# Kernel optimization log

Hardware: AMD Instinct MI355X
Metric: run time of the kernel (lower is better)

Reference implementation:

```python
import jax, jax.numpy as jnp
import numpy as np

SHAPE_MIN = -1.0
SHAPE_LENGTH = 2.0
RESOLUTION = 128
EPS = 1e-05

# plane -> coordinate dims picked by normalize_coordinate
PLANE_DIMS = {"xy": (0, 1), "yz": (1, 2), "xz": (0, 2)}


def setup_inputs() -> dict:
    key = jax.random.key(0)
    k1, k2 = jax.random.split(key)
    B, N, C = 8, 200000, 32
    point_cloud_xyz = jax.random.uniform(k1, (B, N, 3), dtype=jnp.float32, minval=-1.0, maxval=1.0)
    point_cloud_feature = jax.random.normal(k2, (B, C, N), dtype=jnp.float32)
    return {"point_cloud_xyz": point_cloud_xyz, "point_cloud_feature": point_cloud_feature}


def _plane_scatter_mean(xyz_norm, c, plane):
    """xyz_norm: (B,N,3) in [-0.5,0.5]; c: (B,C,N). Returns (B,C,R,R)."""
    R = RESOLUTION
    d0, d1 = PLANE_DIMS[plane]
    xy = jnp.stack([xyz_norm[..., d0], xyz_norm[..., d1]], axis=-1)  # (B,N,2)
    xy = xy / (1.0 + 0.0 + EPS) + 0.5          # padding = 0.0 in generate_plane_features
    xy = jnp.clip(xy, 0.0, 1.0 - EPS)           # normalize_coordinate clamping
    idx = (xy * R).astype(jnp.int32)            # floor via int cast (coords >= 0)
    lin = idx[..., 0] + R * idx[..., 1]         # (B,N) flattened bin index

    def per_batch(cb, ib):
        # cb: (C,N), ib: (N,)
        sums = jax.ops.segment_sum(cb.T, ib, num_segments=R * R)      # (R*R, C)
        cnt = jax.ops.segment_sum(jnp.ones_like(ib, dtype=cb.dtype), ib, num_segments=R * R)
        mean = sums / jnp.maximum(cnt, 1.0)[:, None]                  # empty bins stay 0
        return mean.T.reshape(cb.shape[0], R, R)                      # (C,R,R)

    return jax.vmap(per_batch)(c, lin)


def reference(point_cloud_xyz, point_cloud_feature):
    # map xyz to [-0.5, 0.5] cube
    xyz = (point_cloud_xyz - SHAPE_MIN) / SHAPE_LENGTH - 0.5
    pc_feat_1 = _plane_scatter_mean(xyz, point_cloud_feature, "xy")
    pc_feat_2 = _plane_scatter_mean(xyz, point_cloud_feature, "yz")
    pc_feat_3 = _plane_scatter_mean(xyz, point_cloud_feature, "xz")
    return jnp.stack([pc_feat_1, pc_feat_2, pc_feat_3], axis=1)  # (B,3,C,R,R)
```

## Files before the change

kernel.cpp:

```cpp
#include <hip/hip_runtime.h>


constexpr int R     = 128;
constexpr int NBINS = R * R;
constexpr int NPTS  = 200000;
constexpr int NB    = 8;
constexpr int NC    = 32;
constexpr int SPLIT = 16;
constexpr int TILE  = NPTS / SPLIT;

constexpr size_t OFF_CNTS = 9600000;
constexpr size_t OFF_OFFS = 22182912;
constexpr size_t OFF_OFF  = 102400000;
constexpr size_t OFF_S    = 103972864;
constexpr size_t WS_NEED  = 123172864;

__device__ __forceinline__ int coord_bin(float p) {
    float v = (p + 1.0f) * 0.5f - 0.5f;
    float t = v / 1.00001f + 0.5f;
    t = fminf(fmaxf(t, 0.0f), (float)(1.0 - 1e-5));
    return (int)(t * 128.0f);
}

__global__ __launch_bounds__(256) void bin_kernel(
    const float* __restrict__ xyz, unsigned short* __restrict__ bins) {
    int i = blockIdx.x * 256 + threadIdx.x;
    if (i >= NB * NPTS) return;
    float x = xyz[3 * (size_t)i + 0];
    float y = xyz[3 * (size_t)i + 1];
    float z = xyz[3 * (size_t)i + 2];
    int ix = coord_bin(x), iy = coord_bin(y), iz = coord_bin(z);
    bins[0 * (size_t)NB * NPTS + i] = (unsigned short)(ix + R * iy);
    bins[1 * (size_t)NB * NPTS + i] = (unsigned short)(iy + R * iz);
    bins[2 * (size_t)NB * NPTS + i] = (unsigned short)(ix + R * iz);
}

__global__ __launch_bounds__(1024) void count_kernel(
    const unsigned short* __restrict__ bins, unsigned short* __restrict__ cntS) {
    __shared__ unsigned hist[NBINS];
    int blk   = blockIdx.x;
    int split = blk & (SPLIT - 1);
    int bp    = blk >> 4;
    int b     = bp / 3, plane = bp - 3 * b;
    for (int i = threadIdx.x; i < NBINS; i += 1024) hist[i] = 0u;
    __syncthreads();
    const unsigned* src = (const unsigned*)(bins + ((size_t)plane * NB + b) * NPTS
                                                 + (size_t)split * TILE);
    for (int j = threadIdx.x; j < TILE / 2; j += 1024) {
        unsigned u = src[j];
        atomicAdd(&hist[u & 0xffffu], 1u);
        atomicAdd(&hist[u >> 16], 1u);
    }
    __syncthreads();
    unsigned short* dst = cntS + (size_t)blk * NBINS;
    for (int i = threadIdx.x; i < NBINS; i += 1024)
        dst[i] = (unsigned short)hist[i];
}

__global__ __launch_bounds__(1024) void scan_kernel(
    const unsigned short* __restrict__ cntS, unsigned* __restrict__ off,
    unsigned* __restrict__ offS) {
    __shared__ unsigned tsum[1024];
    int bp = blockIdx.x, t = threadIdx.x;
    const unsigned short* cb = cntS + (size_t)bp * SPLIT * NBINS;
    int base = t * 16;
    unsigned tot[16], v[16];
#pragma unroll
    for (int k = 0; k < 16; ++k) {
        unsigned r = 0;
        for (int s = 0; s < SPLIT; ++s) r += cb[(size_t)s * NBINS + base + k];
        tot[k] = r;
    }
    unsigned run = 0;
#pragma unroll
    for (int k = 0; k < 16; ++k) { v[k] = run; run += tot[k]; }
    tsum[t] = run;
    __syncthreads();
    for (int o = 1; o < 1024; o <<= 1) {
        unsigned a = (t >= o) ? tsum[t - o] : 0u;
        __syncthreads();
        tsum[t] += a;
        __syncthreads();
    }
    unsigned tb = (t > 0) ? tsum[t - 1] : 0u;
    unsigned* ob  = off  + (size_t)bp * NBINS;
    unsigned* osb = offS + (size_t)bp * SPLIT * NBINS;
#pragma unroll
    for (int k = 0; k < 16; ++k) {
        unsigned bb = tb + v[k];
        ob[base + k] = bb;
        unsigned r = 0;
        for (int s = 0; s < SPLIT; ++s) {
            osb[(size_t)s * NBINS + base + k] = bb + r;
            r += cb[(size_t)s * NBINS + base + k];
        }
    }
}

__global__ __launch_bounds__(1024) void reorder_kernel(
    const unsigned short* __restrict__ bins, const unsigned* __restrict__ offS,
    unsigned* __restrict__ S) {
    __shared__ unsigned cur[NBINS];
    int blk   = blockIdx.x;
    int split = blk & (SPLIT - 1);
    int bp    = blk >> 4;
    int b     = bp / 3, plane = bp - 3 * b;
    const unsigned* osb = offS + (size_t)blk * NBINS;
    for (int i = threadIdx.x; i < NBINS; i += 1024) cur[i] = osb[i];
    __syncthreads();
    const unsigned* src = (const unsigned*)(bins + ((size_t)plane * NB + b) * NPTS
                                                 + (size_t)split * TILE);
    unsigned nbase = (unsigned)(split * TILE);
    unsigned* Sp = S + (size_t)bp * NPTS;
    for (int j = threadIdx.x; j < TILE / 2; j += 1024) {
        unsigned u  = src[j];
        unsigned p0 = atomicAdd(&cur[u & 0xffffu], 1u);
        Sp[p0] = nbase + 2 * j;
        unsigned p1 = atomicAdd(&cur[u >> 16], 1u);
        Sp[p1] = nbase + 2 * j + 1;
    }
}

constexpr int TTILES = (NPTS + 255) / 256;
__global__ __launch_bounds__(256) void transpose_kernel(
    const float* __restrict__ feat, unsigned short* __restrict__ ftT) {
    int b = blockIdx.x / TTILES;
    int n = (blockIdx.x % TTILES) * 256 + threadIdx.x;
    if (n >= NPTS) return;
    const float* fb = feat + (size_t)b * NC * NPTS + n;
    unsigned pk[16];
#pragma unroll
    for (int c = 0; c < 16; ++c) {
        unsigned u0 = __float_as_uint(fb[(size_t)(2 * c) * NPTS]);
        unsigned u1 = __float_as_uint(fb[(size_t)(2 * c + 1) * NPTS]);
        unsigned r0 = (u0 + 0x7fffu + ((u0 >> 16) & 1u)) >> 16;
        unsigned r1 = (u1 + 0x7fffu + ((u1 >> 16) & 1u)) >> 16;
        pk[c] = r0 | (r1 << 16);
    }
    uint4* dst = (uint4*)(ftT + ((size_t)b * NPTS + n) * NC);
#pragma unroll
    for (int q = 0; q < 4; ++q)
        dst[q] = make_uint4(pk[4 * q], pk[4 * q + 1], pk[4 * q + 2], pk[4 * q + 3]);
}

__device__ __forceinline__ void accum8(float* acc, uint4 v) {
    acc[0] += __uint_as_float(v.x << 16);
    acc[1] += __uint_as_float(v.x & 0xffff0000u);
    acc[2] += __uint_as_float(v.y << 16);
    acc[3] += __uint_as_float(v.y & 0xffff0000u);
    acc[4] += __uint_as_float(v.z << 16);
    acc[5] += __uint_as_float(v.z & 0xffff0000u);
    acc[6] += __uint_as_float(v.w << 16);
    acc[7] += __uint_as_float(v.w & 0xffff0000u);
}

__global__ __launch_bounds__(256) void gather_kernel(
    const unsigned* __restrict__ off, const unsigned* __restrict__ S,
    const unsigned short* __restrict__ ftT, float* __restrict__ out) {
    int bp  = blockIdx.x >> 6;
    int bin = ((blockIdx.x & 63) << 8) | threadIdx.x;
    int b   = bp / 3;
    const unsigned* op = off + (size_t)bp * NBINS;
    unsigned s = op[bin];
    unsigned e = (bin < NBINS - 1) ? op[bin + 1] : (unsigned)NPTS;
    const unsigned* Sp = S + (size_t)bp * NPTS;
    const unsigned short* fb = ftT + (size_t)b * NPTS * NC;
    float acc[NC];
#pragma unroll
    for (int c = 0; c < NC; ++c) acc[c] = 0.0f;
    unsigned p = s;
    for (; p + 2 <= e; p += 2) {
        unsigned n0 = Sp[p], n1 = Sp[p + 1];
        const uint4* q0 = (const uint4*)(fb + (size_t)n0 * NC);
        const uint4* q1 = (const uint4*)(fb + (size_t)n1 * NC);
        uint4 a0 = q0[0], a1 = q0[1], a2 = q0[2], a3 = q0[3];
        uint4 b0 = q1[0], b1 = q1[1], b2 = q1[2], b3 = q1[3];
        accum8(acc +  0, a0); accum8(acc +  8, a1);
        accum8(acc + 16, a2); accum8(acc + 24, a3);
        accum8(acc +  0, b0); accum8(acc +  8, b1);
        accum8(acc + 16, b2); accum8(acc + 24, b3);
    }
    if (p < e) {
        unsigned n0 = Sp[p];
        const uint4* q0 = (const uint4*)(fb + (size_t)n0 * NC);
        uint4 a0 = q0[0], a1 = q0[1], a2 = q0[2], a3 = q0[3];
        accum8(acc +  0, a0); accum8(acc +  8, a1);
        accum8(acc + 16, a2); accum8(acc + 24, a3);
    }
    float inv = 1.0f / fmaxf((float)(e - s), 1.0f);
    float* ob = out + (size_t)bp * NC * NBINS + bin;
#pragma unroll
    for (int c = 0; c < NC; ++c) ob[(size_t)c * NBINS] = acc[c] * inv;
}

constexpr int CHUNKS = NPTS / 8;
__global__ __launch_bounds__(1024) void count_fb_kernel(
    const unsigned short* __restrict__ bins, unsigned* __restrict__ cnt) {
    __shared__ unsigned hist[NBINS];
    int blk   = blockIdx.x;
    int split = blk & (SPLIT - 1);
    int bp    = blk >> 4;
    int b     = bp / 3, plane = bp - 3 * b;
    for (int i = threadIdx.x; i < NBINS; i += 1024) hist[i] = 0u;
    __syncthreads();
    const unsigned short* src = bins + ((size_t)plane * NB + b) * NPTS
                                     + (size_t)split * TILE;
    for (int n = threadIdx.x; n < TILE; n += 1024) atomicAdd(&hist[src[n]], 1u);
    __syncthreads();
    unsigned* dst = cnt + (size_t)bp * NBINS;
    for (int i = threadIdx.x; i < NBINS; i += 1024) {
        unsigned v = hist[i];
        if (v) atomicAdd(&dst[i], v);
    }
}
__global__ __launch_bounds__(1024) void scatter_kernel(
    const unsigned short* __restrict__ bins, const float* __restrict__ feat,
    const unsigned* __restrict__ cnt, float* __restrict__ out) {
    __shared__ float hist[NBINS];
    int blk = blockIdx.x, b = blk / 96;
    int rem = blk - b * 96, plane = rem >> 5, ch = rem & 31;
    for (int i = threadIdx.x; i < NBINS; i += 1024) hist[i] = 0.0f;
    __syncthreads();
    const uint4*  bp4 = (const uint4*)(bins + ((size_t)plane * NB + b) * NPTS);
    const float4* fp4 = (const float4*)(feat + ((size_t)b * NC + ch) * NPTS);
    for (int p = threadIdx.x; p < CHUNKS; p += 1024) {
        uint4 bb = bp4[p];
        float4 f0 = fp4[2 * p], f1 = fp4[2 * p + 1];
        atomicAdd(&hist[bb.x & 0xffffu], f0.x);
        atomicAdd(&hist[bb.x >> 16],     f0.y);
        atomicAdd(&hist[bb.y & 0xffffu], f0.z);
        atomicAdd(&hist[bb.y >> 16],     f0.w);
        atomicAdd(&hist[bb.z & 0xffffu], f1.x);
        atomicAdd(&hist[bb.z >> 16],     f1.y);
        atomicAdd(&hist[bb.w & 0xffffu], f1.z);
        atomicAdd(&hist[bb.w >> 16],     f1.w);
    }
    __syncthreads();
    const unsigned* cb = cnt + (size_t)(b * 3 + plane) * NBINS;
    float* ob = out + (((size_t)b * 3 + plane) * NC + ch) * (size_t)NBINS;
    for (int i = threadIdx.x; i < NBINS; i += 1024)
        ob[i] = hist[i] / fmaxf((float)cb[i], 1.0f);
}

extern "C" void kernel_launch(void* const* d_in, const int* in_sizes, int n_in,
                              void* d_out, int out_size, void* d_ws, size_t ws_size,
                              hipStream_t stream) {
    const float* xyz  = (const float*)d_in[0];
    const float* feat = (const float*)d_in[1];
    float* out = (float*)d_out;
    char* ws = (char*)d_ws;
    unsigned short* bins = (unsigned short*)ws;

    int total_pts = NB * NPTS;
    bin_kernel<<<(total_pts + 255) / 256, 256, 0, stream>>>(xyz, bins);

    if (ws_size >= WS_NEED) {
        unsigned short* cntS = (unsigned short*)(ws + OFF_CNTS);
        unsigned* offS = (unsigned*)(ws + OFF_OFFS);
        unsigned* off  = (unsigned*)(ws + OFF_OFF);
        unsigned* S    = (unsigned*)(ws + OFF_S);
        unsigned short* ftT = (unsigned short*)ws;
        count_kernel<<<NB * 3 * SPLIT, 1024, 0, stream>>>(bins, cntS);
        scan_kernel<<<NB * 3, 1024, 0, stream>>>(cntS, off, offS);
        reorder_kernel<<<NB * 3 * SPLIT, 1024, 0, stream>>>(bins, offS, S);
        transpose_kernel<<<NB * TTILES, 256, 0, stream>>>(feat, ftT);
        gather_kernel<<<NB * 3 * 64, 256, 0, stream>>>(off, S, ftT, out);
    } else {
        unsigned* cnt = (unsigned*)(ws + OFF_CNTS);
        hipMemsetAsync(cnt, 0, (size_t)NB * 3 * NBINS * sizeof(unsigned), stream);
        count_fb_kernel<<<NB * 3 * SPLIT, 1024, 0, stream>>>(bins, cnt);
        scatter_kernel<<<NB * 3 * NC, 1024, 0, stream>>>(bins, feat, cnt, out);
    }
}
```

Baseline: 527.6 us.

## Replace single-pass counting sort with two-level superbin radix sort

Replaces the 16384-bin counting sort with a two-pass scheme. The first pass counts and scatters into 512 superbins of 32 bins each, packing the sub-bin index into the low bits of each entry. A new per-superbin kernel then sorts locally into the final order and writes the bin offsets. This shrinks the shared-memory histograms and the scan and per-split offset traffic, at the cost of an extra launch and an extra pass over the index array.

```diff
diff --git a/kernel.cpp b/kernel.cpp
--- a/kernel.cpp
+++ b/kernel.cpp
@@ -8,12 +8,16 @@
 constexpr int NC    = 32;
 constexpr int SPLIT = 16;
 constexpr int TILE  = NPTS / SPLIT;
-
-constexpr size_t OFF_CNTS = 9600000;
-constexpr size_t OFF_OFFS = 22182912;
-constexpr size_t OFF_OFF  = 102400000;
-constexpr size_t OFF_S    = 103972864;
-constexpr size_t WS_NEED  = 123172864;
+constexpr int NSB   = 512;
+
+constexpr size_t OFF_SCNT  = 9600000;
+constexpr size_t OFF_SOFFS = 9993216;
+constexpr size_t OFF_S1    = 10779648;
+constexpr size_t OFF_OFF   = 102400000;
+constexpr size_t OFF_S2    = 103972864;
+constexpr size_t OFF_SOFFB = 123172864;
+constexpr size_t WS_NEED   = 123222112;
+constexpr size_t OFF_CNTFB = 9600000;
 
 __device__ __forceinline__ int coord_bin(float p) {
     float v = (p + 1.0f) * 0.5f - 0.5f;
@@ -36,88 +40,111 @@
 }
 
 __global__ __launch_bounds__(1024) void count_kernel(
-    const unsigned short* __restrict__ bins, unsigned short* __restrict__ cntS) {
-    __shared__ unsigned hist[NBINS];
+    const unsigned short* __restrict__ bins, unsigned short* __restrict__ scntS) {
+    __shared__ unsigned h[NSB];
     int blk   = blockIdx.x;
     int split = blk & (SPLIT - 1);
     int bp    = blk >> 4;
     int b     = bp / 3, plane = bp - 3 * b;
-    for (int i = threadIdx.x; i < NBINS; i += 1024) hist[i] = 0u;
+    if (threadIdx.x < NSB) h[threadIdx.x] = 0u;
     __syncthreads();
     const unsigned* src = (const unsigned*)(bins + ((size_t)plane * NB + b) * NPTS
                                                  + (size_t)split * TILE);
     for (int j = threadIdx.x; j < TILE / 2; j += 1024) {
         unsigned u = src[j];
-        atomicAdd(&hist[u & 0xffffu], 1u);
-        atomicAdd(&hist[u >> 16], 1u);
-    }
-    __syncthreads();
-    unsigned short* dst = cntS + (size_t)blk * NBINS;
-    for (int i = threadIdx.x; i < NBINS; i += 1024)
-        dst[i] = (unsigned short)hist[i];
-}
-
-__global__ __launch_bounds__(1024) void scan_kernel(
-    const unsigned short* __restrict__ cntS, unsigned* __restrict__ off,
-    unsigned* __restrict__ offS) {
-    __shared__ unsigned tsum[1024];
+        atomicAdd(&h[(u & 0xffffu) >> 5], 1u);
+        atomicAdd(&h[(u >> 16) >> 5], 1u);
+    }
+    __syncthreads();
+    unsigned short* dst = scntS + (size_t)blk * NSB;
+    if (threadIdx.x < NSB) dst[threadIdx.x] = (unsigned short)h[threadIdx.x];
+}
+
+__global__ __launch_bounds__(512) void sscan_kernel(
+    const unsigned short* __restrict__ scntS, unsigned* __restrict__ soffS,
+    unsigned* __restrict__ soffB) {
+    __shared__ unsigned ts[NSB];
     int bp = blockIdx.x, t = threadIdx.x;
-    const unsigned short* cb = cntS + (size_t)bp * SPLIT * NBINS;
-    int base = t * 16;
-    unsigned tot[16], v[16];
-#pragma unroll
-    for (int k = 0; k < 16; ++k) {
-        unsigned r = 0;
-        for (int s = 0; s < SPLIT; ++s) r += cb[(size_t)s * NBINS + base + k];
-        tot[k] = r;
-    }
+    const unsigned short* cb = scntS + (size_t)bp * SPLIT * NSB;
+    unsigned rel[SPLIT];
     unsigned run = 0;
 #pragma unroll
-    for (int k = 0; k < 16; ++k) { v[k] = run; run += tot[k]; }
-    tsum[t] = run;
-    __syncthreads();
-    for (int o = 1; o < 1024; o <<= 1) {
-        unsigned a = (t >= o) ? tsum[t - o] : 0u;
+    for (int s = 0; s < SPLIT; ++s) {
+        rel[s] = run;
+        run += cb[(size_t)s * NSB + t];
+    }
+    ts[t] = run;
+    __syncthreads();
+    for (int o = 1; o < NSB; o <<= 1) {
+        unsigned a = (t >= o) ? ts[t - o] : 0u;
         __syncthreads();
-        tsum[t] += a;
+        ts[t] += a;
         __syncthreads();
     }
-    unsigned tb = (t > 0) ? tsum[t - 1] : 0u;
-    unsigned* ob  = off  + (size_t)bp * NBINS;
-    unsigned* osb = offS + (size_t)bp * SPLIT * NBINS;
-#pragma unroll
-    for (int k = 0; k < 16; ++k) {
-        unsigned bb = tb + v[k];
-        ob[base + k] = bb;
-        unsigned r = 0;
-        for (int s = 0; s < SPLIT; ++s) {
-            osb[(size_t)s * NBINS + base + k] = bb + r;
-            r += cb[(size_t)s * NBINS + base + k];
-        }
-    }
+    unsigned base = ts[t] - run;
+    unsigned* osb = soffS + (size_t)bp * SPLIT * NSB;
+#pragma unroll
+    for (int s = 0; s < SPLIT; ++s) osb[(size_t)s * NSB + t] = base + rel[s];
+    soffB[bp * 513 + t] = base;
+    if (t == NSB - 1) soffB[bp * 513 + NSB] = ts[t];
 }
 
 __global__ __launch_bounds__(1024) void reorder_kernel(
-    const unsigned short* __restrict__ bins, const unsigned* __restrict__ offS,
-    unsigned* __restrict__ S) {
-    __shared__ unsigned cur[NBINS];
+    const unsigned short* __restrict__ bins, const unsigned* __restrict__ soffS,
+    unsigned* __restrict__ S1) {
+    __shared__ unsigned cur[NSB];
     int blk   = blockIdx.x;
     int split = blk & (SPLIT - 1);
     int bp    = blk >> 4;
     int b     = bp / 3, plane = bp - 3 * b;
-    const unsigned* osb = offS + (size_t)blk * NBINS;
-    for (int i = threadIdx.x; i < NBINS; i += 1024) cur[i] = osb[i];
+    const unsigned* osb = soffS + (size_t)blk * NSB;
+    if (threadIdx.x < NSB) cur[threadIdx.x] = osb[threadIdx.x];
     __syncthreads();
     const unsigned* src = (const unsigned*)(bins + ((size_t)plane * NB + b) * NPTS
                                                  + (size_t)split * TILE);
     unsigned nbase = (unsigned)(split * TILE);
-    unsigned* Sp = S + (size_t)bp * NPTS;
+    unsigned* ep = S1 + (size_t)bp * NPTS;
     for (int j = threadIdx.x; j < TILE / 2; j += 1024) {
         unsigned u  = src[j];
-        unsigned p0 = atomicAdd(&cur[u & 0xffffu], 1u);
-        Sp[p0] = nbase + 2 * j;
-        unsigned p1 = atomicAdd(&cur[u >> 16], 1u);
-        Sp[p1] = nbase + 2 * j + 1;
+        unsigned l0 = u & 0xffffu, l1 = u >> 16;
+        unsigned p0 = atomicAdd(&cur[l0 >> 5], 1u);
+        ep[p0] = ((nbase + 2u * j) << 5) | (l0 & 31u);
+        unsigned p1 = atomicAdd(&cur[l1 >> 5], 1u);
+        ep[p1] = ((nbase + 2u * j + 1u) << 5) | (l1 & 31u);
+    }
+}
+
+__global__ __launch_bounds__(64) void localsort_kernel(
+    const unsigned* __restrict__ soffB, const unsigned* __restrict__ S1,
+    unsigned* __restrict__ off, unsigned* __restrict__ S2) {
+    __shared__ unsigned cnt[32], cur[32];
+    int bp = blockIdx.x >> 9;
+    int sb = blockIdx.x & 511;
+    int t  = threadIdx.x;
+    unsigned s = soffB[bp * 513 + sb], e = soffB[bp * 513 + sb + 1];
+    if (t < 32) cnt[t] = 0u;
+    __syncthreads();
+    const unsigned* S1p = S1 + (size_t)bp * NPTS;
+    for (unsigned j = s + t; j < e; j += 64)
+        atomicAdd(&cnt[S1p[j] & 31u], 1u);
+    __syncthreads();
+    unsigned v = (t < 32) ? cnt[t] : 0u;
+#pragma unroll
+    for (int o = 1; o < 32; o <<= 1) {
+        unsigned u = __shfl_up(v, o, 32);
+        if ((t & 31) >= o) v += u;
+    }
+    if (t < 32) {
+        unsigned excl = v - cnt[t];
+        cur[t] = excl;
+        off[(size_t)bp * NBINS + sb * 32 + t] = s + excl;
+    }
+    __syncthreads();
+    unsigned* S2p = S2 + (size_t)bp * NPTS;
+    for (unsigned j = s + t; j < e; j += 64) {
+        unsigned en = S1p[j];
+        unsigned p  = atomicAdd(&cur[en & 31u], 1u);
+        S2p[s + p] = en >> 5;
     }
 }
 
@@ -155,7 +182,7 @@
 }
 
 __global__ __launch_bounds__(256) void gather_kernel(
-    const unsigned* __restrict__ off, const unsigned* __restrict__ S,
+    const unsigned* __restrict__ off, const unsigned* __restrict__ S2,
     const unsigned short* __restrict__ ftT, float* __restrict__ out) {
     int bp  = blockIdx.x >> 6;
     int bin = ((blockIdx.x & 63) << 8) | threadIdx.x;
@@ -163,7 +190,7 @@
     const unsigned* op = off + (size_t)bp * NBINS;
     unsigned s = op[bin];
     unsigned e = (bin < NBINS - 1) ? op[bin + 1] : (unsigned)NPTS;
-    const unsigned* Sp = S + (size_t)bp * NPTS;
+    const unsigned* Sp = S2 + (size_t)bp * NPTS;
     const unsigned short* fb = ftT + (size_t)b * NPTS * NC;
     float acc[NC];
 #pragma unroll
@@ -255,18 +282,21 @@
     bin_kernel<<<(total_pts + 255) / 256, 256, 0, stream>>>(xyz, bins);
 
     if (ws_size >= WS_NEED) {
-        unsigned short* cntS = (unsigned short*)(ws + OFF_CNTS);
-        unsigned* offS = (unsigned*)(ws + OFF_OFFS);
-        unsigned* off  = (unsigned*)(ws + OFF_OFF);
-        unsigned* S    = (unsigned*)(ws + OFF_S);
+        unsigned short* scntS = (unsigned short*)(ws + OFF_SCNT);
+        unsigned* soffS = (unsigned*)(ws + OFF_SOFFS);
+        unsigned* S1    = (unsigned*)(ws + OFF_S1);
+        unsigned* off   = (unsigned*)(ws + OFF_OFF);
+        unsigned* S2    = (unsigned*)(ws + OFF_S2);
+        unsigned* soffB = (unsigned*)(ws + OFF_SOFFB);
         unsigned short* ftT = (unsigned short*)ws;
-        count_kernel<<<NB * 3 * SPLIT, 1024, 0, stream>>>(bins, cntS);
-        scan_kernel<<<NB * 3, 1024, 0, stream>>>(cntS, off, offS);
-        reorder_kernel<<<NB * 3 * SPLIT, 1024, 0, stream>>>(bins, offS, S);
+        count_kernel<<<NB * 3 * SPLIT, 1024, 0, stream>>>(bins, scntS);
+        sscan_kernel<<<NB * 3, 512, 0, stream>>>(scntS, soffS, soffB);
+        reorder_kernel<<<NB * 3 * SPLIT, 1024, 0, stream>>>(bins, soffS, S1);
+        localsort_kernel<<<NB * 3 * NSB, 64, 0, stream>>>(soffB, S1, off, S2);
         transpose_kernel<<<NB * TTILES, 256, 0, stream>>>(feat, ftT);
-        gather_kernel<<<NB * 3 * 64, 256, 0, stream>>>(off, S, ftT, out);
+        gather_kernel<<<NB * 3 * 64, 256, 0, stream>>>(off, S2, ftT, out);
     } else {
-        unsigned* cnt = (unsigned*)(ws + OFF_CNTS);
+        unsigned* cnt = (unsigned*)(ws + OFF_CNTFB);
         hipMemsetAsync(cnt, 0, (size_t)NB * 3 * NBINS * sizeof(unsigned), stream);
         count_fb_kernel<<<NB * 3 * SPLIT, 1024, 0, stream>>>(bins, cnt);
         scatter_kernel<<<NB * 3 * NC, 1024, 0, stream>>>(bins, feat, cnt, out);
```

Result: faster. 455.6 us (-13.6%).
